# Performance work log

Measured on AMD Instinct MI355X. Metric: run time of the kernel, lower is better.

The kernel has to match this reference:

```python
import jax, jax.numpy as jnp
import numpy as np


def _elu_feature_map(x):
    return jax.nn.elu(x) + 1.0


def setup_inputs() -> dict:
    key = jax.random.key(0)
    kq, kk, kv = jax.random.split(key, 3)
    shape = (4, 4096, 8, 64)  # n, s, h, d
    Q = jax.random.normal(kq, shape, dtype=jnp.float32)
    K = jax.random.normal(kk, shape, dtype=jnp.float32)
    V = jax.random.normal(kv, shape, dtype=jnp.float32)
    return {"Q": Q, "K": K, "V": V}


def reference(Q, K, V):
    eps = 1e-06
    Qf = _elu_feature_map(Q)  # [n,l,h,d]
    Kf = _elu_feature_map(K)  # [n,s,h,d]
    v_length = V.shape[1]
    Vn = V / v_length  # normalize values for numerical stability
    # KV: [n,h,d,v] -- sum over sequence of K outer V
    KV = jnp.einsum('nshd,nshv->nhdv', Kf, Vn)
    # Z: inverse normalizer [n,l,h]
    Z = 1.0 / (jnp.einsum('nlhd,nhd->nlh', Qf, Kf.sum(axis=1)) + eps)
    out = jnp.einsum('nlhd,nhdv,nlh->nlhv', Qf, KV, Z) * v_length
    return out
```

## Files before the change

### kernel.cpp

```cpp
#include <hip/hip_runtime.h>
#include <math.h>

#define SEQ 4096
#define NH  8
#define DIM 64

__device__ __forceinline__ float elu1(float x) {
    return __expf(fminf(x, 0.0f)) + fmaxf(x, 0.0f);
}

__global__ __launch_bounds__(256) void k_phase1(const float* __restrict__ Kin,
                                                const float* __restrict__ Vin,
                                                float* __restrict__ pKV,
                                                float* __restrict__ pKs,
                                                int NC, int sLen) {
    const int nh = blockIdx.x / NC;
    const int ck = blockIdx.x % NC;
    const int n  = nh >> 3, h = nh & 7;
    const int t  = threadIdx.x;
    const int r  = t >> 4;
    const int c4 = (t & 15) * 4;
    const int wv = t >> 6, lane = t & 63;
    const int d0 = (lane >> 3) * 8;
    const int v0 = (lane & 7) * 8;

    __shared__ __align__(16) float kf[4096];
    __shared__ __align__(16) float vv[4096];

    float acc[8][8];
#pragma unroll
    for (int i = 0; i < 8; i++)
#pragma unroll
        for (int j = 0; j < 8; j++) acc[i][j] = 0.0f;
    float ksl[4] = {0.f, 0.f, 0.f, 0.f};

    const size_t base = ((size_t)(n * SEQ + ck * sLen) * NH + h) * DIM;
    const int ntiles = sLen >> 6;

    for (int tile = 0; tile < ntiles; ++tile) {
        if (tile) __syncthreads();
        const float* Kb = Kin + base + ((size_t)tile * 64 + r) * (NH * DIM) + c4;
        const float* Vb = Vin + base + ((size_t)tile * 64 + r) * (NH * DIM) + c4;
        float4 kreg[4], vreg[4];
#pragma unroll
        for (int i = 0; i < 4; ++i) {
            kreg[i] = *(const float4*)(Kb + (size_t)i * 16 * (NH * DIM));
            vreg[i] = *(const float4*)(Vb + (size_t)i * 16 * (NH * DIM));
        }
#pragma unroll
        for (int i = 0; i < 4; ++i) {
            float4 f4;
            f4.x = elu1(kreg[i].x); f4.y = elu1(kreg[i].y);
            f4.z = elu1(kreg[i].z); f4.w = elu1(kreg[i].w);
            ksl[0] += f4.x; ksl[1] += f4.y; ksl[2] += f4.z; ksl[3] += f4.w;
            *(float4*)&kf[(r + 16 * i) * 64 + c4] = f4;
            *(float4*)&vv[(r + 16 * i) * 64 + c4] = vreg[i];
        }
        __syncthreads();
#pragma unroll 2
        for (int ssi = 0; ssi < 16; ++ssi) {
            const int ss = wv * 16 + ssi;
            float4 a0 = *(const float4*)&kf[ss * 64 + d0];
            float4 a1 = *(const float4*)&kf[ss * 64 + d0 + 4];
            float4 b0 = *(const float4*)&vv[ss * 64 + v0];
            float4 b1 = *(const float4*)&vv[ss * 64 + v0 + 4];
            float a[8] = {a0.x, a0.y, a0.z, a0.w, a1.x, a1.y, a1.z, a1.w};
            float b[8] = {b0.x, b0.y, b0.z, b0.w, b1.x, b1.y, b1.z, b1.w};
#pragma unroll
            for (int i = 0; i < 8; i++)
#pragma unroll
                for (int j = 0; j < 8; j++)
                    acc[i][j] = fmaf(a[i], b[j], acc[i][j]);
        }
    }
    __syncthreads();

#define ACC_W(S) { _Pragma("unroll") for (int i_=0;i_<8;i_++) _Pragma("unroll") for (int j_=0;j_<8;j_++) (S)[(i_*8+j_)*64+lane]=acc[i_][j_]; }
#define ACC_A(S) { _Pragma("unroll") for (int i_=0;i_<8;i_++) _Pragma("unroll") for (int j_=0;j_<8;j_++) acc[i_][j_]+=(S)[(i_*8+j_)*64+lane]; }
    if (wv == 1) ACC_W(kf);
    if (wv == 3) ACC_W(vv);
    __syncthreads();
    if (wv == 0) ACC_A(kf);
    if (wv == 2) ACC_A(vv);
    __syncthreads();
    if (wv == 2) ACC_W(kf);
    __syncthreads();
    if (wv == 0) {
        ACC_A(kf);
        const int pnh = n * 8 + h;
        float* dst = pKV + ((size_t)ck * 32 + pnh) * 4096;
#pragma unroll
        for (int i = 0; i < 8; i++) {
            float4 oa, ob;
            oa.x = acc[i][0]; oa.y = acc[i][1]; oa.z = acc[i][2]; oa.w = acc[i][3];
            ob.x = acc[i][4]; ob.y = acc[i][5]; ob.z = acc[i][6]; ob.w = acc[i][7];
            *(float4*)(dst + (d0 + i) * 64 + v0)     = oa;
            *(float4*)(dst + (d0 + i) * 64 + v0 + 4) = ob;
        }
    }
    *(float4*)&vv[r * 64 + c4] = make_float4(ksl[0], ksl[1], ksl[2], ksl[3]);
    __syncthreads();
    if (t < 64) {
        float s = 0.0f;
#pragma unroll
        for (int rr = 0; rr < 16; ++rr) s += vv[rr * 64 + t];
        pKs[((size_t)ck * 32 + n * 8 + h) * 64 + t] = s;
    }
}

template <int NC>
__global__ __launch_bounds__(128) void k_reduceT(const float* __restrict__ pKV,
                                                 const float* __restrict__ pKs,
                                                 float* __restrict__ KVf,
                                                 float* __restrict__ Ksf) {
    const int gid = blockIdx.x * 128 + threadIdx.x;
    const float4* p4 = (const float4*)pKV;
    float4 s = make_float4(0.f, 0.f, 0.f, 0.f);
#pragma unroll
    for (int c = 0; c < NC; ++c) {
        float4 v = p4[(size_t)c * 32768 + gid];
        s.x += v.x; s.y += v.y; s.z += v.z; s.w += v.w;
    }
    ((float4*)KVf)[gid] = s;
    if (gid < 2048) {
        float ss = 0.0f;
#pragma unroll
        for (int c = 0; c < NC; ++c) ss += pKs[(size_t)c * 2048 + gid];
        Ksf[gid] = ss;
    }
}

__global__ __launch_bounds__(128) void k_reduceG(const float* __restrict__ pKV,
                                                 const float* __restrict__ pKs,
                                                 float* __restrict__ KVf,
                                                 float* __restrict__ Ksf, int NC) {
    const int gid = blockIdx.x * 128 + threadIdx.x;
    const float4* p4 = (const float4*)pKV;
    float4 s = make_float4(0.f, 0.f, 0.f, 0.f);
    for (int c = 0; c < NC; ++c) {
        float4 v = p4[(size_t)c * 32768 + gid];
        s.x += v.x; s.y += v.y; s.z += v.z; s.w += v.w;
    }
    ((float4*)KVf)[gid] = s;
    if (gid < 2048) {
        float ss = 0.0f;
        for (int c = 0; c < NC; ++c) ss += pKs[(size_t)c * 2048 + gid];
        Ksf[gid] = ss;
    }
}

__global__ __launch_bounds__(256) void k_phase2(const float* __restrict__ Qin,
                                                const float* __restrict__ KVf,
                                                const float* __restrict__ Ksf,
                                                float* __restrict__ Out) {
    const int nh   = blockIdx.x >> 4;
    const int tile = blockIdx.x & 15;
    const int n = nh >> 3, h = nh & 7;
    const int t = threadIdx.x;

    __shared__ __align__(16) float Qt[16 * 256];
    __shared__ __align__(16) float KVs[64][64];
    __shared__ float Kss[64];

    {
        const float4* src = (const float4*)(KVf + (size_t)nh * 4096);
        float4* dst = (float4*)&KVs[0][0];
#pragma unroll
        for (int i = 0; i < 4; ++i) dst[t + 256 * i] = src[t + 256 * i];
        if (t < 64) Kss[t] = Ksf[nh * 64 + t];
    }

    const int l0 = tile * 256;
    const int r0 = (t >> 3) * 8;
    const int v0 = (t & 7) * 8;

    float acc[8][8];
#pragma unroll
    for (int i = 0; i < 8; i++)
#pragma unroll
        for (int j = 0; j < 8; j++) acc[i][j] = 0.0f;
    float p[8] = {0.f, 0.f, 0.f, 0.f, 0.f, 0.f, 0.f, 0.f};

    for (int dc = 0; dc < 4; ++dc) {
        if (dc) __syncthreads();
#pragma unroll
        for (int i = 0; i < 4; ++i) {
            const int j   = t + 256 * i;
            const int row = j >> 2;
            const int dl4 = (j & 3) << 2;
            const size_t g = ((size_t)(n * SEQ + l0 + row) * NH + h) * DIM + dc * 16 + dl4;
            float4 q4 = *(const float4*)(Qin + g);
            const int col = row ^ dl4;
            Qt[(dl4 + 0) * 256 + col] = elu1(q4.x);
            Qt[(dl4 + 1) * 256 + col] = elu1(q4.y);
            Qt[(dl4 + 2) * 256 + col] = elu1(q4.z);
            Qt[(dl4 + 3) * 256 + col] = elu1(q4.w);
        }
        __syncthreads();

#pragma unroll 2
        for (int dl = 0; dl < 16; ++dl) {
            const int d = dc * 16 + dl;
            const int s = dl & 12;
            float4 qa = *(const float4*)&Qt[dl * 256 + (r0 ^ s)];
            float4 qb = *(const float4*)&Qt[dl * 256 + ((r0 + 4) ^ s)];
            float4 ka = *(const float4*)&KVs[d][v0];
            float4 kb = *(const float4*)&KVs[d][v0 + 4];
            const float ksd = Kss[d];
            float q[8]  = {qa.x, qa.y, qa.z, qa.w, qb.x, qb.y, qb.z, qb.w};
            float kv[8] = {ka.x, ka.y, ka.z, ka.w, kb.x, kb.y, kb.z, kb.w};
#pragma unroll
            for (int i = 0; i < 8; ++i) {
                p[i] = fmaf(q[i], ksd, p[i]);
#pragma unroll
                for (int jj = 0; jj < 8; ++jj)
                    acc[i][jj] = fmaf(q[i], kv[jj], acc[i][jj]);
            }
        }
    }

#pragma unroll
    for (int i = 0; i < 8; ++i) {
        const float z = 1.0f / (p[i] + 1e-6f);
        const int l = l0 + r0 + i;
        float* o = Out + ((size_t)(n * SEQ + l) * NH + h) * DIM + v0;
        float4 oa, ob;
        oa.x = acc[i][0] * z; oa.y = acc[i][1] * z; oa.z = acc[i][2] * z; oa.w = acc[i][3] * z;
        ob.x = acc[i][4] * z; ob.y = acc[i][5] * z; ob.z = acc[i][6] * z; ob.w = acc[i][7] * z;
        *(float4*)(o)     = oa;
        *(float4*)(o + 4) = ob;
    }
}

extern "C" void kernel_launch(void* const* d_in, const int* in_sizes, int n_in,
                              void* d_out, int out_size, void* d_ws, size_t ws_size,
                              hipStream_t stream) {
    const float* Q = (const float*)d_in[0];
    const float* K = (const float*)d_in[1];
    const float* V = (const float*)d_in[2];
    float* out = (float*)d_out;

    int NC = 16;
    const size_t unit = 133120ull * 4ull;
    while (NC > 1 && (size_t)(NC + 1) * unit > ws_size) NC >>= 1;
    const int sLen = SEQ / NC;

    float* KVf = (float*)d_ws;
    float* Ksf = KVf + 32 * 4096;
    float* pKV = Ksf + 32 * 64;
    float* pKs = pKV + (size_t)NC * 32 * 4096;

    hipLaunchKernelGGL(k_phase1, dim3(32 * NC), dim3(256), 0, stream, K, V, pKV, pKs, NC, sLen);
    switch (NC) {
        case 16: hipLaunchKernelGGL(k_reduceT<16>, dim3(256), dim3(128), 0, stream, pKV, pKs, KVf, Ksf); break;
        case 8:  hipLaunchKernelGGL(k_reduceT<8>,  dim3(256), dim3(128), 0, stream, pKV, pKs, KVf, Ksf); break;
        case 4:  hipLaunchKernelGGL(k_reduceT<4>,  dim3(256), dim3(128), 0, stream, pKV, pKs, KVf, Ksf); break;
        default: hipLaunchKernelGGL(k_reduceG, dim3(256), dim3(128), 0, stream, pKV, pKs, KVf, Ksf, NC); break;
    }
    hipLaunchKernelGGL(k_phase2, dim3(512), dim3(256), 0, stream, Q, KVf, Ksf, out);
}
```

Before: 56.41 us.

## Double-buffer K/V tiles in LDS to overlap global loads with FMA compute

```diff
diff --git a/kernel.cpp b/kernel.cpp
--- a/kernel.cpp
+++ b/kernel.cpp
@@ -23,9 +23,10 @@
     const int wv = t >> 6, lane = t & 63;
     const int d0 = (lane >> 3) * 8;
     const int v0 = (lane & 7) * 8;
-
-    __shared__ __align__(16) float kf[4096];
-    __shared__ __align__(16) float vv[4096];
+    const int RS = NH * DIM;
+
+    __shared__ __align__(16) float kf[2][4096];
+    __shared__ __align__(16) float vv[2][4096];
 
     float acc[8][8];
 #pragma unroll
@@ -37,33 +38,42 @@
     const size_t base = ((size_t)(n * SEQ + ck * sLen) * NH + h) * DIM;
     const int ntiles = sLen >> 6;
 
+    {
+        const float* Kb = Kin + base + (size_t)r * RS + c4;
+        const float* Vb = Vin + base + (size_t)r * RS + c4;
+#pragma unroll
+        for (int i = 0; i < 4; ++i) {
+            float4 k4 = *(const float4*)(Kb + (size_t)(16 * i) * RS);
+            float4 v4 = *(const float4*)(Vb + (size_t)(16 * i) * RS);
+            float4 f4;
+            f4.x = elu1(k4.x); f4.y = elu1(k4.y); f4.z = elu1(k4.z); f4.w = elu1(k4.w);
+            ksl[0] += f4.x; ksl[1] += f4.y; ksl[2] += f4.z; ksl[3] += f4.w;
+            *(float4*)&kf[0][(r + 16 * i) * 64 + c4] = f4;
+            *(float4*)&vv[0][(r + 16 * i) * 64 + c4] = v4;
+        }
+    }
+
+    int cur = 0;
     for (int tile = 0; tile < ntiles; ++tile) {
-        if (tile) __syncthreads();
-        const float* Kb = Kin + base + ((size_t)tile * 64 + r) * (NH * DIM) + c4;
-        const float* Vb = Vin + base + ((size_t)tile * 64 + r) * (NH * DIM) + c4;
+        __syncthreads();
         float4 kreg[4], vreg[4];
-#pragma unroll
-        for (int i = 0; i < 4; ++i) {
-            kreg[i] = *(const float4*)(Kb + (size_t)i * 16 * (NH * DIM));
-            vreg[i] = *(const float4*)(Vb + (size_t)i * 16 * (NH * DIM));
-        }
-#pragma unroll
-        for (int i = 0; i < 4; ++i) {
-            float4 f4;
-            f4.x = elu1(kreg[i].x); f4.y = elu1(kreg[i].y);
-            f4.z = elu1(kreg[i].z); f4.w = elu1(kreg[i].w);
-            ksl[0] += f4.x; ksl[1] += f4.y; ksl[2] += f4.z; ksl[3] += f4.w;
-            *(float4*)&kf[(r + 16 * i) * 64 + c4] = f4;
-            *(float4*)&vv[(r + 16 * i) * 64 + c4] = vreg[i];
-        }
-        __syncthreads();
+        const bool more = (tile + 1 < ntiles);
+        if (more) {
+            const float* Kb = Kin + base + ((size_t)((tile + 1) * 64) + r) * RS + c4;
+            const float* Vb = Vin + base + ((size_t)((tile + 1) * 64) + r) * RS + c4;
+#pragma unroll
+            for (int i = 0; i < 4; ++i) {
+                kreg[i] = *(const float4*)(Kb + (size_t)(16 * i) * RS);
+                vreg[i] = *(const float4*)(Vb + (size_t)(16 * i) * RS);
+            }
+        }
 #pragma unroll 2
         for (int ssi = 0; ssi < 16; ++ssi) {
             const int ss = wv * 16 + ssi;
-            float4 a0 = *(const float4*)&kf[ss * 64 + d0];
-            float4 a1 = *(const float4*)&kf[ss * 64 + d0 + 4];
-            float4 b0 = *(const float4*)&vv[ss * 64 + v0];
-            float4 b1 = *(const float4*)&vv[ss * 64 + v0 + 4];
+            float4 a0 = *(const float4*)&kf[cur][ss * 64 + d0];
+            float4 a1 = *(const float4*)&kf[cur][ss * 64 + d0 + 4];
+            float4 b0 = *(const float4*)&vv[cur][ss * 64 + v0];
+            float4 b1 = *(const float4*)&vv[cur][ss * 64 + v0 + 4];
             float a[8] = {a0.x, a0.y, a0.z, a0.w, a1.x, a1.y, a1.z, a1.w};
             float b[8] = {b0.x, b0.y, b0.z, b0.w, b1.x, b1.y, b1.z, b1.w};
 #pragma unroll
@@ -72,21 +82,34 @@
                 for (int j = 0; j < 8; j++)
                     acc[i][j] = fmaf(a[i], b[j], acc[i][j]);
         }
+        if (more) {
+#pragma unroll
+            for (int i = 0; i < 4; ++i) {
+                float4 f4;
+                f4.x = elu1(kreg[i].x); f4.y = elu1(kreg[i].y);
+                f4.z = elu1(kreg[i].z); f4.w = elu1(kreg[i].w);
+                ksl[0] += f4.x; ksl[1] += f4.y; ksl[2] += f4.z; ksl[3] += f4.w;
+                *(float4*)&kf[cur ^ 1][(r + 16 * i) * 64 + c4] = f4;
+                *(float4*)&vv[cur ^ 1][(r + 16 * i) * 64 + c4] = vreg[i];
+            }
+            cur ^= 1;
+        }
     }
     __syncthreads();
 
 #define ACC_W(S) { _Pragma("unroll") for (int i_=0;i_<8;i_++) _Pragma("unroll") for (int j_=0;j_<8;j_++) (S)[(i_*8+j_)*64+lane]=acc[i_][j_]; }
 #define ACC_A(S) { _Pragma("unroll") for (int i_=0;i_<8;i_++) _Pragma("unroll") for (int j_=0;j_<8;j_++) acc[i_][j_]+=(S)[(i_*8+j_)*64+lane]; }
-    if (wv == 1) ACC_W(kf);
-    if (wv == 3) ACC_W(vv);
-    __syncthreads();
-    if (wv == 0) ACC_A(kf);
-    if (wv == 2) ACC_A(vv);
-    __syncthreads();
-    if (wv == 2) ACC_W(kf);
+    if (wv == 1) ACC_W(kf[0]);
+    if (wv == 3) ACC_W(kf[1]);
+    *(float4*)&vv[0][r * 64 + c4] = make_float4(ksl[0], ksl[1], ksl[2], ksl[3]);
+    __syncthreads();
+    if (wv == 0) ACC_A(kf[0]);
+    if (wv == 2) ACC_A(kf[1]);
+    __syncthreads();
+    if (wv == 2) ACC_W(kf[0]);
     __syncthreads();
     if (wv == 0) {
-        ACC_A(kf);
+        ACC_A(kf[0]);
         const int pnh = n * 8 + h;
         float* dst = pKV + ((size_t)ck * 32 + pnh) * 4096;
 #pragma unroll
@@ -98,12 +121,10 @@
             *(float4*)(dst + (d0 + i) * 64 + v0 + 4) = ob;
         }
     }
-    *(float4*)&vv[r * 64 + c4] = make_float4(ksl[0], ksl[1], ksl[2], ksl[3]);
-    __syncthreads();
     if (t < 64) {
         float s = 0.0f;
 #pragma unroll
-        for (int rr = 0; rr < 16; ++rr) s += vv[rr * 64 + t];
+        for (int rr = 0; rr < 16; ++rr) s += vv[0][rr * 64 + t];
         pKs[((size_t)ck * 32 + n * 8 + h) * 64 + t] = s;
     }
 }
```

Measured after the change: 78.43 us. 1.39x slower.
